# Kernel tuning notes

Hardware: AMD Instinct MI355X
Metric: run time of the kernel (lower is better)

Reference implementation:

```python
import jax, jax.numpy as jnp
import numpy as np

N, M, D = 2048, 16, 256


def setup_inputs() -> dict:
    key = jax.random.key(0)
    k1, = jax.random.split(key, 1)
    embeddings = jax.random.normal(k1, (N, M, D), dtype=jnp.float32)
    w = jnp.asarray(10.0, dtype=jnp.float32)
    b = jnp.asarray(-5.0, dtype=jnp.float32)
    return {"embeddings": embeddings, "w": w, "b": b}


def reference(embeddings, w, b):
    # embeddings: [N, M, D]
    centroids = embeddings.mean(axis=1)          # [N, D]
    sum_ = embeddings.sum(axis=1)                # [N, D]
    e = embeddings.reshape(N * M, D)             # [NM, D]
    cosine_sim = e @ centroids.T                 # [NM, N]
    # excluded-self centroid for each (speaker j, utterance i):
    # cj = (sum_[j] - e_ji) / (M - 1); replace cosine_sim[ji, j] with dot(cj, e_ji)
    excl = (sum_[:, None, :] - embeddings) / (M - 1)           # [N, M, D]
    diag_vals = jnp.sum(excl * embeddings, axis=-1).reshape(N * M)  # [NM]
    labels = jnp.repeat(jnp.arange(N), M)                      # [NM]
    cosine_sim = cosine_sim.at[jnp.arange(N * M), labels].set(diag_vals)
    logits = w * cosine_sim + b                                # [NM, N]
    logp = jax.nn.log_softmax(logits, axis=-1)
    loss = -jnp.mean(logp[jnp.arange(N * M), labels])
    return loss
```

## Files before the change

### kernel.cpp

```cpp
#include <hip/hip_runtime.h>
#include <hip/hip_bf16.h>
#if !__has_builtin(__builtin_amdgcn_cvt_pk_fp8_f32)
#include <hip/hip_fp8.h>
#endif

#define NS 2048
#define MU 16
#define DD 256
#define NMROWS (NS*MU)
#define STRIPS 8
#define SC 256
#define NSTEP 4
#define BMROWS 256
#define THR 8.0f

typedef float  f32x4  __attribute__((ext_vector_type(4)));
typedef float  f32x16 __attribute__((ext_vector_type(16)));
typedef int    i32x4  __attribute__((ext_vector_type(4)));

#define LOG2E 1.44269504088896340736f
#define LN2   0.69314718055994530942f

#if __has_builtin(__builtin_amdgcn_exp2f)
#define EXP2F(x) __builtin_amdgcn_exp2f(x)
#else
#define EXP2F(x) exp2f(x)
#endif
#if __has_builtin(__builtin_amdgcn_logf)
#define LOG2F(x) __builtin_amdgcn_logf(x)
#else
#define LOG2F(x) __log2f(x)
#endif

__device__ __forceinline__ int pk4(float a, float b, float c, float d){
#if __has_builtin(__builtin_amdgcn_cvt_pk_fp8_f32)
  int v = __builtin_amdgcn_cvt_pk_fp8_f32(a, b, 0, false);
  v = __builtin_amdgcn_cvt_pk_fp8_f32(c, d, v, true);
  return v;
#else
  unsigned r = (unsigned)__hip_fp8_e4m3(a).__x
             | ((unsigned)__hip_fp8_e4m3(b).__x << 8)
             | ((unsigned)__hip_fp8_e4m3(c).__x << 16)
             | ((unsigned)__hip_fp8_e4m3(d).__x << 24);
  return (int)r;
#endif
}
__device__ __forceinline__ long mk64(int lo, int hi){
  return (long)(((unsigned long long)(unsigned)lo) |
                ((unsigned long long)(unsigned)hi << 32));
}


__launch_bounds__(256)
__global__ void prep_kernel(const float* __restrict__ emb,
                            const float* __restrict__ wp,
                            long* __restrict__ centk8,
                            unsigned char* __restrict__ embk8,
                            float* __restrict__ diag2){
  __shared__ float E[16*260];
  __shared__ float sm[256];
  const int t = threadIdx.x;
  const int n = blockIdx.x;
  const float* src = emb + (size_t)n*MU*DD;

  #pragma unroll
  for (int i=0;i<4;i++){
    int g = i*1024 + t*4;
    f32x4 v = *(const f32x4*)(src + g);
    int m = g >> 8, d = g & 255;
    *(f32x4*)&E[m*260 + d] = v;
  }
  __syncthreads();

  {
    float s = 0.f;
    #pragma unroll
    for (int m=0;m<16;m++) s += E[m*260 + t];
    sm[t] = s;
  }
  __syncthreads();

  const float w2 = wp[0] * LOG2E;

  if (t < 16){
    const float c16 = w2 * (1.0f/16.0f);
    const int st = t;
    const float* p = &sm[st*16];
    int q0 = pk4(p[0]*c16,  p[1]*c16,  p[2]*c16,  p[3]*c16);
    int q1 = pk4(p[4]*c16,  p[5]*c16,  p[6]*c16,  p[7]*c16);
    int q2 = pk4(p[8]*c16,  p[9]*c16,  p[10]*c16, p[11]*c16);
    int q3 = pk4(p[12]*c16, p[13]*c16, p[14]*c16, p[15]*c16);
    size_t base = ((size_t)(st*64 + (n>>5))*2)*32 + (n&31);
    centk8[base]      = mk64(q0, q1);
    centk8[base + 32] = mk64(q2, q3);
  }

  if (embk8){
    int st = t >> 4, r = t & 15;
    const float* p = &E[r*260 + st*16];
    i32x4 o;
    #pragma unroll
    for (int q=0;q<4;q++){
      f32x4 v = *(const f32x4*)(p + q*4);
      o[q] = pk4(v[0], v[1], v[2], v[3]);
    }
    *(i32x4*)(embk8 + ((size_t)st*NMROWS + n*16 + r)*16) = o;
  }

  {
    int m = t >> 4, j = t & 15;
    float acc = 0.f;
    #pragma unroll
    for (int i=0;i<16;i++){
      int d = j + 16*i;
      float e = E[m*260 + d];
      acc += e * (sm[d] - e);
    }
    acc += __shfl_xor(acc, 1, 16);
    acc += __shfl_xor(acc, 2, 16);
    acc += __shfl_xor(acc, 4, 16);
    acc += __shfl_xor(acc, 8, 16);
    if (j==0) diag2[n*16 + m] = acc * (w2 * (1.0f/15.0f));
  }
}

__device__ __forceinline__ void stage_strip(const long* __restrict__ centk8,
                                            long* lds, int cg0,
                                            int wave, int lane){
  #pragma unroll
  for (int i=0;i<8;i++){
    const int L  = wave*8 + i;
    const int st = L >> 2;
    const int q  = L & 3;
    const long* g = centk8 + (size_t)(st*64 + cg0)*64 + q*128 + lane*2;
    __builtin_amdgcn_global_load_lds(
        (const __attribute__((address_space(1))) void*)g,
        (__attribute__((address_space(3))) void*)(lds + (size_t)st*512 + q*128),
        16, 0, 0);
  }
}

#define MFMA8(a,b,c) __builtin_amdgcn_mfma_f32_32x32x16_fp8_fp8(a,b,c,0,0,0)

template<bool FROMF32>
__launch_bounds__(512,4)
__global__ void ge2e_main(const float* __restrict__ embf,
                          const unsigned char* __restrict__ embk8,
                          const long* __restrict__ centk8,
                          const float* __restrict__ diag2,
                          float2* __restrict__ msbuf){
  __shared__ long Bs[8192];

  const int tid  = threadIdx.x;
  const int lane = tid & 63;
  const int wave = tid >> 6;
  const int l31  = lane & 31, hi = lane >> 5;
  const int strip  = blockIdx.x & 7;
  const int rowBlk = blockIdx.x >> 3;
  const int c0 = strip * SC;
  const int rowA = rowBlk*BMROWS + wave*32 + l31;

  stage_strip(centk8, Bs, c0 >> 5, wave, lane);

  long af[16];
  if constexpr (FROMF32){
    const float* rp = embf + (size_t)rowA*DD;
    #pragma unroll
    for (int st=0; st<16; ++st){
      f32x4 v0 = *(const f32x4*)(rp + 16*st + 8*hi);
      f32x4 v1 = *(const f32x4*)(rp + 16*st + 8*hi + 4);
      af[st] = mk64(pk4(v0[0],v0[1],v0[2],v0[3]), pk4(v1[0],v1[1],v1[2],v1[3]));
    }
  } else {
    #pragma unroll
    for (int st=0; st<16; ++st)
      af[st] = *(const long*)(embk8 + ((size_t)st*NMROWS + rowA)*16 + hi*8);
  }

  const float dv  = diag2[rowA];
  const int   lab = rowA >> 4;
  const int   labc0 = rowBlk*16;
  const bool  hasdiag = (labc0 >= c0) && (labc0 < c0 + SC);
  const int   dstep = (labc0 - c0) >> 6;
  const int   dgrp  = ((labc0 - c0) >> 5) & 1;

  float mneg = 0.f, s = 0.f;

  __syncthreads();

  #pragma unroll
  for (int step=0; step<NSTEP; ++step){
    f32x16 ci;
    #pragma unroll
    for (int i=0;i<16;i++) ci[i] = mneg;

    f32x16 accA, accB;
    {
      const long bA = Bs[(size_t)((0*8 + step*2    )*2 + hi)*32 + l31];
      const long bB = Bs[(size_t)((0*8 + step*2 + 1)*2 + hi)*32 + l31];
      accA = MFMA8(bA, af[0], ci);
      accB = MFMA8(bB, af[0], ci);
    }
    #pragma unroll
    for (int st=1; st<16; ++st){
      const long bA = Bs[(size_t)((st*8 + step*2    )*2 + hi)*32 + l31];
      const long bB = Bs[(size_t)((st*8 + step*2 + 1)*2 + hi)*32 + l31];
      accA = MFMA8(bA, af[st], accA);
      accB = MFMA8(bB, af[st], accB);
    }

    if (hasdiag && step == dstep){
      int colbase = c0 + step*64 + dgrp*32 + 4*hi;
      if (dgrp == 0){
        #pragma unroll
        for (int r=0;r<16;r++){
          int col = colbase + (r&3) + 8*(r>>2);
          if (col == lab) accA[r] = dv + mneg;
        }
      } else {
        #pragma unroll
        for (int r=0;r<16;r++){
          int col = colbase + (r&3) + 8*(r>>2);
          if (col == lab) accB[r] = dv + mneg;
        }
      }
    }

    float xa0 = fmaxf(fmaxf(fmaxf(accA[0],accA[1]),fmaxf(accA[2],accA[3])),
                      fmaxf(fmaxf(accA[4],accA[5]),fmaxf(accA[6],accA[7])));
    float xa1 = fmaxf(fmaxf(fmaxf(accA[8],accA[9]),fmaxf(accA[10],accA[11])),
                      fmaxf(fmaxf(accA[12],accA[13]),fmaxf(accA[14],accA[15])));
    float xb0 = fmaxf(fmaxf(fmaxf(accB[0],accB[1]),fmaxf(accB[2],accB[3])),
                      fmaxf(fmaxf(accB[4],accB[5]),fmaxf(accB[6],accB[7])));
    float xb1 = fmaxf(fmaxf(fmaxf(accB[8],accB[9]),fmaxf(accB[10],accB[11])),
                      fmaxf(fmaxf(accB[12],accB[13]),fmaxf(accB[14],accB[15])));
    float tm = fmaxf(fmaxf(xa0,xa1), fmaxf(xb0,xb1));

    if (__any(tm > THR)){
      float d = fmaxf(tm, 0.f);
      s *= EXP2F(-d);
      mneg -= d;
      float a0=0.f, b0=0.f;
      #pragma unroll
      for (int r=0;r<16;r++){ a0 += EXP2F(accA[r]-d); b0 += EXP2F(accB[r]-d); }
      s += a0 + b0;
    } else {
      float a0 = EXP2F(accA[0])+EXP2F(accA[1])+EXP2F(accA[2])+EXP2F(accA[3]);
      float a1 = EXP2F(accA[4])+EXP2F(accA[5])+EXP2F(accA[6])+EXP2F(accA[7]);
      float a2 = EXP2F(accA[8])+EXP2F(accA[9])+EXP2F(accA[10])+EXP2F(accA[11]);
      float a3 = EXP2F(accA[12])+EXP2F(accA[13])+EXP2F(accA[14])+EXP2F(accA[15]);
      float b0 = EXP2F(accB[0])+EXP2F(accB[1])+EXP2F(accB[2])+EXP2F(accB[3]);
      float b1 = EXP2F(accB[4])+EXP2F(accB[5])+EXP2F(accB[6])+EXP2F(accB[7]);
      float b2 = EXP2F(accB[8])+EXP2F(accB[9])+EXP2F(accB[10])+EXP2F(accB[11]);
      float b3 = EXP2F(accB[12])+EXP2F(accB[13])+EXP2F(accB[14])+EXP2F(accB[15]);
      s += ((a0+a1)+(a2+a3)) + ((b0+b1)+(b2+b3));
    }
  }

  float m  = -mneg;
  float mo = __shfl_xor(m,32,64), so = __shfl_xor(s,32,64);
  float mm = fmaxf(m,mo);
  float ss = s*EXP2F(m-mm) + so*EXP2F(mo-mm);

  if (hi==0) msbuf[(size_t)strip*NMROWS + rowA] = make_float2(mm, ss);
}

__launch_bounds__(512)
__global__ void merge_kernel(const float2* __restrict__ msbuf,
                             const float* __restrict__ diag2,
                             float* __restrict__ partials){
  __shared__ float sh[8];
  const int row = blockIdx.x*512 + threadIdx.x;
  float2 p[STRIPS];
  #pragma unroll
  for (int k=0;k<STRIPS;k++) p[k] = msbuf[(size_t)k*NMROWS + row];
  float mm = p[0].x;
  #pragma unroll
  for (int k=1;k<STRIPS;k++) mm = fmaxf(mm, p[k].x);
  float ss = 0.f;
  #pragma unroll
  for (int k=0;k<STRIPS;k++) ss += p[k].y * EXP2F(p[k].x - mm);
  float term = LN2*(mm + LOG2F(ss) - diag2[row]);
  #pragma unroll
  for (int off=32; off; off>>=1) term += __shfl_xor(term, off, 64);
  if ((threadIdx.x & 63)==0) sh[threadIdx.x>>6] = term;
  __syncthreads();
  if (threadIdx.x==0){
    float v = 0.f;
    #pragma unroll
    for (int i=0;i<8;i++) v += sh[i];
    partials[blockIdx.x] = v;
  }
}

__global__ void final_kernel(const float* __restrict__ partials,
                             float* __restrict__ out){
  int tid = threadIdx.x;
  float v = partials[tid];
  #pragma unroll
  for (int off=32; off; off>>=1) v += __shfl_xor(v, off, 64);
  if (tid==0) out[0] = v * (1.0f/NMROWS);
}

extern "C" void kernel_launch(void* const* d_in, const int* in_sizes, int n_in,
                              void* d_out, int out_size, void* d_ws, size_t ws_size,
                              hipStream_t stream){
  const float* emb = (const float*)d_in[0];
  const float* wp  = (const float*)d_in[1];
  float* out = (float*)d_out;
  char* ws = (char*)d_ws;

  const size_t centk_b = (size_t)NS*DD;
  const size_t embk_b  = (size_t)NMROWS*DD;
  const size_t diag_b  = (size_t)NMROWS*4;
  const size_t ms_b    = (size_t)STRIPS*NMROWS*8;
  const bool useEmbk = ws_size >= centk_b + embk_b + diag_b + ms_b + 1024;

  long* centk8 = (long*)ws;
  size_t off = centk_b;
  unsigned char* embk8 = useEmbk ? (unsigned char*)(ws + off) : nullptr;
  if (useEmbk) off += embk_b;
  float*  diag2 = (float*)(ws + off);  off += diag_b;
  float2* msbuf = (float2*)(ws + off); off += ms_b;
  float*  parts = (float*)(ws + off);

  prep_kernel<<<NS, 256, 0, stream>>>(emb, wp, centk8, embk8, diag2);
  if (useEmbk)
    ge2e_main<false><<<(NMROWS/BMROWS)*STRIPS, 512, 0, stream>>>(emb, embk8, centk8, diag2, msbuf);
  else
    ge2e_main<true><<<(NMROWS/BMROWS)*STRIPS, 512, 0, stream>>>(emb, embk8, centk8, diag2, msbuf);
  merge_kernel<<<NMROWS/512, 512, 0, stream>>>(msbuf, diag2, parts);
  final_kernel<<<1, 64, 0, stream>>>(parts, out);
}
```

Baseline: 50.86 us.

## Switch to scaled 32x32x64 FP8 MFMA with double-buffered centroid staging

Replaces the 32x32x16 FP8 MFMA with the MI355X scaled 32x32x64 f8f6f4 MFMA (unit scales), which cuts the MFMA instruction count per K by four. The centroid layout becomes 16-byte chunks per column and K-strip. The column tile is staged per 64-column step into double-buffered LDS, overlapping the next global-to-LDS load with compute. The block shrinks to 256 threads and 128 rows, doubling the grid, and each step now ends with a vmcnt wait and a barrier, which adds sync overhead.

```diff
diff --git a/kernel.cpp b/kernel.cpp
--- a/kernel.cpp
+++ b/kernel.cpp
@@ -11,12 +11,13 @@
 #define STRIPS 8
 #define SC 256
 #define NSTEP 4
-#define BMROWS 256
+#define BMROWS 128
 #define THR 8.0f
 
 typedef float  f32x4  __attribute__((ext_vector_type(4)));
 typedef float  f32x16 __attribute__((ext_vector_type(16)));
 typedef int    i32x4  __attribute__((ext_vector_type(4)));
+typedef int    i32x8  __attribute__((ext_vector_type(8)));
 
 #define LOG2E 1.44269504088896340736f
 #define LN2   0.69314718055994530942f
@@ -45,16 +46,12 @@
   return (int)r;
 #endif
 }
-__device__ __forceinline__ long mk64(int lo, int hi){
-  return (long)(((unsigned long long)(unsigned)lo) |
-                ((unsigned long long)(unsigned)hi << 32));
-}
 
 
 __launch_bounds__(256)
 __global__ void prep_kernel(const float* __restrict__ emb,
                             const float* __restrict__ wp,
-                            long* __restrict__ centk8,
+                            i32x4* __restrict__ centk16,
                             unsigned char* __restrict__ embk8,
                             float* __restrict__ diag2){
   __shared__ float E[16*260];
@@ -86,13 +83,11 @@
     const float c16 = w2 * (1.0f/16.0f);
     const int st = t;
     const float* p = &sm[st*16];
-    int q0 = pk4(p[0]*c16,  p[1]*c16,  p[2]*c16,  p[3]*c16);
-    int q1 = pk4(p[4]*c16,  p[5]*c16,  p[6]*c16,  p[7]*c16);
-    int q2 = pk4(p[8]*c16,  p[9]*c16,  p[10]*c16, p[11]*c16);
-    int q3 = pk4(p[12]*c16, p[13]*c16, p[14]*c16, p[15]*c16);
-    size_t base = ((size_t)(st*64 + (n>>5))*2)*32 + (n&31);
-    centk8[base]      = mk64(q0, q1);
-    centk8[base + 32] = mk64(q2, q3);
+    i32x4 o;
+    #pragma unroll
+    for (int q=0;q<4;q++)
+      o[q] = pk4(p[q*4]*c16, p[q*4+1]*c16, p[q*4+2]*c16, p[q*4+3]*c16);
+    centk16[(size_t)st*NS + n] = o;
   }
 
   if (embk8){
@@ -124,32 +119,31 @@
   }
 }
 
-__device__ __forceinline__ void stage_strip(const long* __restrict__ centk8,
-                                            long* lds, int cg0,
-                                            int wave, int lane){
-  #pragma unroll
-  for (int i=0;i<8;i++){
-    const int L  = wave*8 + i;
-    const int st = L >> 2;
-    const int q  = L & 3;
-    const long* g = centk8 + (size_t)(st*64 + cg0)*64 + q*128 + lane*2;
+__device__ __forceinline__ void stage_b(const i32x4* __restrict__ centk16,
+                                        i32x4* lds, int col0,
+                                        int wave, int lane){
+  #pragma unroll
+  for (int i=0;i<4;i++){
+    const int st = i*4 + wave;
+    const i32x4* g = centk16 + (size_t)st*NS + col0 + lane;
     __builtin_amdgcn_global_load_lds(
         (const __attribute__((address_space(1))) void*)g,
-        (__attribute__((address_space(3))) void*)(lds + (size_t)st*512 + q*128),
+        (__attribute__((address_space(3))) void*)(lds + (size_t)st*64),
         16, 0, 0);
   }
 }
 
-#define MFMA8(a,b,c) __builtin_amdgcn_mfma_f32_32x32x16_fp8_fp8(a,b,c,0,0,0)
+#define MFMAS(a,b,c) __builtin_amdgcn_mfma_scale_f32_32x32x64_f8f6f4( \
+    a, b, c, 0, 0, 0, 0x7f7f7f7fu, 0, 0x7f7f7f7fu)
 
 template<bool FROMF32>
-__launch_bounds__(512,4)
+__launch_bounds__(256,4)
 __global__ void ge2e_main(const float* __restrict__ embf,
                           const unsigned char* __restrict__ embk8,
-                          const long* __restrict__ centk8,
+                          const i32x4* __restrict__ centk16,
                           const float* __restrict__ diag2,
                           float2* __restrict__ msbuf){
-  __shared__ long Bs[8192];
+  __shared__ i32x4 Bbuf[2][1024];
 
   const int tid  = threadIdx.x;
   const int lane = tid & 63;
@@ -160,26 +154,37 @@
   const int c0 = strip * SC;
   const int rowA = rowBlk*BMROWS + wave*32 + l31;
 
-  stage_strip(centk8, Bs, c0 >> 5, wave, lane);
-
-  long af[16];
+  stage_b(centk16, &Bbuf[0][0], c0, wave, lane);
+
+  i32x8 af[4];
   if constexpr (FROMF32){
     const float* rp = embf + (size_t)rowA*DD;
     #pragma unroll
-    for (int st=0; st<16; ++st){
-      f32x4 v0 = *(const f32x4*)(rp + 16*st + 8*hi);
-      f32x4 v1 = *(const f32x4*)(rp + 16*st + 8*hi + 4);
-      af[st] = mk64(pk4(v0[0],v0[1],v0[2],v0[3]), pk4(v1[0],v1[1],v1[2],v1[3]));
+    for (int c=0;c<4;c++){
+      i32x8 o;
+      #pragma unroll
+      for (int h=0;h<2;h++){
+        const float* q = rp + (4*c + 2*hi + h)*16;
+        #pragma unroll
+        for (int j=0;j<4;j++)
+          o[h*4+j] = pk4(q[j*4], q[j*4+1], q[j*4+2], q[j*4+3]);
+      }
+      af[c] = o;
     }
   } else {
     #pragma unroll
-    for (int st=0; st<16; ++st)
-      af[st] = *(const long*)(embk8 + ((size_t)st*NMROWS + rowA)*16 + hi*8);
+    for (int c=0;c<4;c++){
+      i32x4 x = *(const i32x4*)(embk8 + ((size_t)(4*c+2*hi  )*NMROWS + rowA)*16);
+      i32x4 y = *(const i32x4*)(embk8 + ((size_t)(4*c+2*hi+1)*NMROWS + rowA)*16);
+      i32x8 o; o[0]=x[0];o[1]=x[1];o[2]=x[2];o[3]=x[3];
+               o[4]=y[0];o[5]=y[1];o[6]=y[2];o[7]=y[3];
+      af[c] = o;
+    }
   }
 
   const float dv  = diag2[rowA];
   const int   lab = rowA >> 4;
-  const int   labc0 = rowBlk*16;
+  const int   labc0 = rowBlk*8;
   const bool  hasdiag = (labc0 >= c0) && (labc0 < c0 + SC);
   const int   dstep = (labc0 - c0) >> 6;
   const int   dgrp  = ((labc0 - c0) >> 5) & 1;
@@ -188,25 +193,30 @@
 
   __syncthreads();
 
-  #pragma unroll
   for (int step=0; step<NSTEP; ++step){
+    const int cb_ = step & 1;
+    if (step+1 < NSTEP)
+      stage_b(centk16, &Bbuf[cb_^1][0], c0 + (step+1)*64, wave, lane);
+
+    const i32x4* cur = &Bbuf[cb_][0];
+
     f32x16 ci;
     #pragma unroll
     for (int i=0;i<16;i++) ci[i] = mneg;
 
-    f32x16 accA, accB;
-    {
-      const long bA = Bs[(size_t)((0*8 + step*2    )*2 + hi)*32 + l31];
-      const long bB = Bs[(size_t)((0*8 + step*2 + 1)*2 + hi)*32 + l31];
-      accA = MFMA8(bA, af[0], ci);
-      accB = MFMA8(bB, af[0], ci);
-    }
-    #pragma unroll
-    for (int st=1; st<16; ++st){
-      const long bA = Bs[(size_t)((st*8 + step*2    )*2 + hi)*32 + l31];
-      const long bB = Bs[(size_t)((st*8 + step*2 + 1)*2 + hi)*32 + l31];
-      accA = MFMA8(bA, af[st], accA);
-      accB = MFMA8(bB, af[st], accB);
+    f32x16 accA = ci, accB = ci;
+    #pragma unroll
+    for (int c=0;c<4;c++){
+      i32x4 a0 = cur[(4*c+2*hi  )*64      + l31];
+      i32x4 a1 = cur[(4*c+2*hi+1)*64      + l31];
+      i32x4 b0 = cur[(4*c+2*hi  )*64 + 32 + l31];
+      i32x4 b1 = cur[(4*c+2*hi+1)*64 + 32 + l31];
+      i32x8 bA; bA[0]=a0[0];bA[1]=a0[1];bA[2]=a0[2];bA[3]=a0[3];
+                bA[4]=a1[0];bA[5]=a1[1];bA[6]=a1[2];bA[7]=a1[3];
+      i32x8 bB; bB[0]=b0[0];bB[1]=b0[1];bB[2]=b0[2];bB[3]=b0[3];
+                bB[4]=b1[0];bB[5]=b1[1];bB[6]=b1[2];bB[7]=b1[3];
+      accA = MFMAS(bA, af[c], accA);
+      accB = MFMAS(bB, af[c], accB);
     }
 
     if (hasdiag && step == dstep){
@@ -255,6 +265,9 @@
       float b3 = EXP2F(accB[12])+EXP2F(accB[13])+EXP2F(accB[14])+EXP2F(accB[15]);
       s += ((a0+a1)+(a2+a3)) + ((b0+b1)+(b2+b3));
     }
+
+    asm volatile("s_waitcnt vmcnt(0)" ::: "memory");
+    __builtin_amdgcn_s_barrier();
   }
 
   float m  = -mneg;
@@ -316,7 +329,7 @@
   const size_t ms_b    = (size_t)STRIPS*NMROWS*8;
   const bool useEmbk = ws_size >= centk_b + embk_b + diag_b + ms_b + 1024;
 
-  long* centk8 = (long*)ws;
+  i32x4* centk16 = (i32x4*)ws;
   size_t off = centk_b;
   unsigned char* embk8 = useEmbk ? (unsigned char*)(ws + off) : nullptr;
   if (useEmbk) off += embk_b;
@@ -324,11 +337,11 @@
   float2* msbuf = (float2*)(ws + off); off += ms_b;
   float*  parts = (float*)(ws + off);
 
-  prep_kernel<<<NS, 256, 0, stream>>>(emb, wp, centk8, embk8, diag2);
+  prep_kernel<<<NS, 256, 0, stream>>>(emb, wp, centk16, embk8, diag2);
   if (useEmbk)
-    ge2e_main<false><<<(NMROWS/BMROWS)*STRIPS, 512, 0, stream>>>(emb, embk8, centk8, diag2, msbuf);
+    ge2e_main<false><<<(NMROWS/BMROWS)*STRIPS, 256, 0, stream>>>(emb, embk8, centk16, diag2, msbuf);
   else
-    ge2e_main<true><<<(NMROWS/BMROWS)*STRIPS, 512, 0, stream>>>(emb, embk8, centk8, diag2, msbuf);
+    ge2e_main<true><<<(NMROWS/BMROWS)*STRIPS, 256, 0, stream>>>(emb, embk8, centk16, diag2, msbuf);
   merge_kernel<<<NMROWS/512, 512, 0, stream>>>(msbuf, diag2, parts);
   final_kernel<<<1, 64, 0, stream>>>(parts, out);
 }
```

New measurement: 41.61 us. -18.2%, faster.
